# Performance work log

Hardware: AMD Instinct MI355X
Metric: run time of the kernel (lower is better)

The kernel has to match this reference:

```python
import jax, jax.numpy as jnp
import numpy as np

B, H, L, P = 16, 256, 8192, 64  # batch, d_input, seq_len, d_state


def setup_inputs() -> dict:
    key = jax.random.key(0)
    k1, k2, k3, k4, k5, k6 = jax.random.split(key, 6)
    u = jax.random.normal(k1, (B, H, L), dtype=jnp.float32)
    # diagonal SSM poles on an annulus inside the unit disk (stable discrete dynamics)
    radius = jax.random.uniform(k2, (P,), minval=0.5, maxval=0.99)
    theta = jax.random.uniform(k3, (P,), minval=0.0, maxval=2.0 * np.pi)
    A_re = (radius * jnp.cos(theta)).astype(jnp.float32)
    A_im = (radius * jnp.sin(theta)).astype(jnp.float32)
    # combined input/output mixing W = C*B, complex (H, P)
    BC_re = (jax.random.normal(k4, (H, P)) / np.sqrt(P)).astype(jnp.float32)
    BC_im = (jax.random.normal(k5, (H, P)) / np.sqrt(P)).astype(jnp.float32)
    # D skip vector: uniform_ring(min_radius=0.0, max_radius=1.0, field='real')
    D = jax.random.uniform(k6, (H,), minval=0.0, maxval=1.0, dtype=jnp.float32)
    return {"u": u, "A_re": A_re, "A_im": A_im, "BC_re": BC_re, "BC_im": BC_im, "D": D}


def reference(u, A_re, A_im, BC_re, BC_im, D):
    # Vandermonde kernel: k[h, l] = sum_p BC[h, p] * A[p]**l, computed stably via exp(l*log A)
    A = jax.lax.complex(A_re, A_im)                      # (P,)
    logA = jnp.log(A)                                    # (P,) complex
    ell = jnp.arange(L, dtype=jnp.float32)               # (L,)
    V = jnp.exp(logA[:, None] * ell[None, :])            # (P, L) complex Vandermonde
    BC = jax.lax.complex(BC_re, BC_im)                   # (H, P)
    k = jnp.einsum('hp,pl->hl', BC, V)                   # (H, L) complex kernel
    # circular FFT convolution (same-length fft/ifft as the torch code)
    u_s = jnp.fft.fft(u, axis=-1)                        # (B, H, L) complex
    k_s = jnp.fft.fft(k, axis=-1)                        # (H, L) complex
    y = jnp.fft.ifft(u_s * k_s[None, :, :], axis=-1).real
    y = y + D[None, :, None] * u                         # D*u skip
    return jnp.tanh(y)                                   # activation (dropout=0 -> identity)
```

## Files before the change

### kernel.cpp

```cpp
#include <hip/hip_runtime.h>
#include <cmath>


typedef _Float16 half8 __attribute__((ext_vector_type(8)));
typedef _Float16 half4v __attribute__((ext_vector_type(4)));
typedef float floatx16 __attribute__((ext_vector_type(16)));

#define NC 64
#define CM 128
#define A2_BYTES ((size_t)256 * 128 * 256 * 2)
#define W_BYTES  ((size_t)128 * 128 * 2)
#define AM_OFF   (A2_BYTES + W_BYTES)

#define SWH(r, c) ((((r) << 7)) | ((c) ^ (((r) & 15) << 3)))

__device__ __forceinline__ float fast_tanh(float x) {
    float e2 = __expf(2.0f * x);
    return 1.0f - 2.0f / (e2 + 1.0f);
}

__global__ void fftconv_prep(const float* __restrict__ A_re, const float* __restrict__ A_im,
                             const float* __restrict__ BC_re, const float* __restrict__ BC_im,
                             const float* __restrict__ Dv, char* __restrict__ ws) {
    __shared__ float rr[64], th[64], br[64], bi[64];
    __shared__ float kk[CM];
    const int h = blockIdx.x, tid = threadIdx.x;
    if (tid < 64) {
        float x = A_re[tid], y = A_im[tid];
        rr[tid] = log2f(sqrtf(x * x + y * y));
        th[tid] = atan2f(y, x);
        br[tid] = BC_re[h * 64 + tid];
        bi[tid] = BC_im[h * 64 + tid];
    }
    __syncthreads();
    if (tid < CM) {
        float d = (float)tid, s = 0.f;
        for (int p = 0; p < 64; ++p) {
            float mag = exp2f(d * rr[p]);
            float ang = d * th[p];
            s += mag * (br[p] * cosf(ang) - bi[p] * sinf(ang));
        }
        kk[tid] = s;
    }
    __syncthreads();
    _Float16* A2 = (_Float16*)ws + (size_t)h * 128 * 256;
    const float Dh = Dv[h];
    for (int idx = tid; idx < 128 * 128; idx += 256) {
        int r = idx >> 7, pc = idx & 127, p = pc & 63;
        float e = (float)(r + 1);
        float mag = exp2f(e * rr[p]);
        float ang = e * th[p];
        float cr = mag * cosf(ang), ci = mag * sinf(ang);
        float val = (pc < 64) ? (br[p] * cr - bi[p] * ci) : -(br[p] * ci + bi[p] * cr);
        A2[r * 256 + pc] = (_Float16)val;
    }
    for (int idx = tid; idx < 128 * 128; idx += 256) {
        int r = idx >> 7, j = idx & 127;
        float v = (j <= r) ? kk[r - j] : 0.f;
        if (j == r) v += Dh;
        A2[r * 256 + CM + j] = (_Float16)v;
    }
    if (h == 0) {
        _Float16* W = (_Float16*)(ws + A2_BYTES);
        for (int idx = tid; idx < 128 * 128; idx += 256) {
            int pc = idx >> 7, j = idx & 127, p = pc & 63;
            float e = (float)(127 - j);
            float mag = exp2f(e * rr[p]);
            float ang = e * th[p];
            float v = (pc < 64) ? mag * cosf(ang) : mag * sinf(ang);
            W[pc * 128 + j] = (_Float16)v;
        }
        if (tid < 64) {
            float mag = exp2f(128.f * rr[tid]);
            float ang = 128.f * th[tid];
            float* aM = (float*)(ws + AM_OFF);
            aM[tid] = mag * cosf(ang);
            aM[64 + tid] = mag * sinf(ang);
        }
    }
}

__global__ __launch_bounds__(256, 4)
void fftconv_main(const float* __restrict__ u, const char* __restrict__ ws,
                  float* __restrict__ out) {
    __shared__ __align__(16) _Float16 u16[NC * CM];
    __shared__ __align__(16) _Float16 S16[NC * CM];

    const int tid = threadIdx.x;
    const int lane = tid & 63;
    const int wv = tid >> 6;
    const int h = blockIdx.x >> 4;
    const int bb = blockIdx.x & 15;
    const float* ub = u + ((size_t)bb * 256 + h) * 8192;
    float* yb = out + ((size_t)bb * 256 + h) * 8192;

    const int mrow = (wv << 5) + (lane & 31);
    const int kh = (lane >> 5) << 3;
    const int ncol = lane & 31;

    const _Float16* Wg = (const _Float16*)(ws + A2_BYTES) + (size_t)mrow * CM + kh;
    const _Float16* Ag = (const _Float16*)ws + ((size_t)h * CM + mrow) * 256 + kh;

    float4 uv[8];
#pragma unroll
    for (int i = 0; i < 8; ++i) uv[i] = ((const float4*)ub)[i * 256 + tid];
    half8 wf[8];
#pragma unroll
    for (int s = 0; s < 8; ++s) wf[s] = *(const half8*)(Wg + (s << 4));

#pragma unroll
    for (int i = 0; i < 8; ++i) {
        int e4 = i * 256 + tid;
        int c = e4 >> 5, j = (e4 << 2) & 127;
        half4v hv = { (_Float16)uv[i].x, (_Float16)uv[i].y,
                      (_Float16)uv[i].z, (_Float16)uv[i].w };
        *(half4v*)&u16[SWH(c, j)] = hv;
    }
    __syncthreads();

    {
        floatx16 acc0 = {}; floatx16 acc1 = {};
#pragma unroll
        for (int s = 0; s < 8; ++s) {
            int k0 = (s << 4) + kh;
            half8 b0 = *(const half8*)&u16[SWH(ncol, k0)];
            half8 b1 = *(const half8*)&u16[SWH(ncol + 32, k0)];
            acc0 = __builtin_amdgcn_mfma_f32_32x32x16_f16(wf[s], b0, acc0, 0, 0, 0);
            acc1 = __builtin_amdgcn_mfma_f32_32x32x16_f16(wf[s], b1, acc1, 0, 0, 0);
        }
        const int pc0 = (wv << 5) + ((lane >> 5) << 2);
#pragma unroll
        for (int g = 0; g < 4; ++g) {
            half4v h0 = { (_Float16)acc0[4 * g + 0], (_Float16)acc0[4 * g + 1],
                          (_Float16)acc0[4 * g + 2], (_Float16)acc0[4 * g + 3] };
            *(half4v*)&S16[SWH(ncol, pc0 + 8 * g)] = h0;
            half4v h1 = { (_Float16)acc1[4 * g + 0], (_Float16)acc1[4 * g + 1],
                          (_Float16)acc1[4 * g + 2], (_Float16)acc1[4 * g + 3] };
            *(half4v*)&S16[SWH(ncol + 32, pc0 + 8 * g)] = h1;
        }
    }
    half8 gf[8];
#pragma unroll
    for (int s = 0; s < 8; ++s) gf[s] = *(const half8*)(Ag + (s << 4));
    __syncthreads();

    {
        const float* aM = (const float*)(ws + AM_OFF);
        const float amr = aM[lane], ami = aM[64 + lane];
        float prd[8], pid[8];
        prd[0] = 1.f; pid[0] = 0.f;
#pragma unroll
        for (int d = 1; d < 8; ++d) {
            prd[d] = prd[d - 1] * amr - pid[d - 1] * ami;
            pid[d] = prd[d - 1] * ami + pid[d - 1] * amr;
        }
        const int cbase = wv << 4;
        float sr = 0.f, si = 0.f;
#pragma unroll
        for (int d = 0; d < 8; ++d) {
            int cc = (cbase - 1 - d) & 63;
            float xr = (float)S16[SWH(cc, lane)];
            float xi = (float)S16[SWH(cc, 64 + lane)];
            sr = fmaf(prd[d], xr, fmaf(-pid[d], xi, sr));
            si = fmaf(prd[d], xi, fmaf(pid[d], xr, si));
        }
        float er[16], ei[16];
        er[0] = sr; ei[0] = si;
#pragma unroll
        for (int i = 1; i < 16; ++i) {
            int cc = cbase + i - 1;
            float xr = (float)S16[SWH(cc, lane)];
            float xi = (float)S16[SWH(cc, 64 + lane)];
            float nr = fmaf(amr, sr, fmaf(-ami, si, xr));
            float ni = fmaf(amr, si, fmaf(ami, sr, xi));
            sr = nr; si = ni; er[i] = sr; ei[i] = si;
        }
        __syncthreads();
#pragma unroll
        for (int i = 0; i < 16; ++i) {
            int c = cbase + i;
            S16[SWH(c, lane)] = (_Float16)er[i];
            S16[SWH(c, 64 + lane)] = (_Float16)ei[i];
        }
    }
    half8 tf[8];
#pragma unroll
    for (int s = 0; s < 8; ++s) tf[s] = *(const half8*)(Ag + CM + (s << 4));
    __syncthreads();

    {
        floatx16 acc0 = {}; floatx16 acc1 = {};
#pragma unroll
        for (int s = 0; s < 8; ++s) {
            int k0 = (s << 4) + kh;
            half8 b0 = *(const half8*)&S16[SWH(ncol, k0)];
            half8 b1 = *(const half8*)&S16[SWH(ncol + 32, k0)];
            acc0 = __builtin_amdgcn_mfma_f32_32x32x16_f16(gf[s], b0, acc0, 0, 0, 0);
            acc1 = __builtin_amdgcn_mfma_f32_32x32x16_f16(gf[s], b1, acc1, 0, 0, 0);
        }
#pragma unroll
        for (int s = 0; s < 8; ++s) {
            int k0 = (s << 4) + kh;
            half8 b0 = *(const half8*)&u16[SWH(ncol, k0)];
            half8 b1 = *(const half8*)&u16[SWH(ncol + 32, k0)];
            acc0 = __builtin_amdgcn_mfma_f32_32x32x16_f16(tf[s], b0, acc0, 0, 0, 0);
            acc1 = __builtin_amdgcn_mfma_f32_32x32x16_f16(tf[s], b1, acc1, 0, 0, 0);
        }
        const int r0 = (wv << 5) + ((lane >> 5) << 2);
#pragma unroll
        for (int g = 0; g < 4; ++g) {
            float4 o0;
            o0.x = fast_tanh(acc0[4 * g + 0]); o0.y = fast_tanh(acc0[4 * g + 1]);
            o0.z = fast_tanh(acc0[4 * g + 2]); o0.w = fast_tanh(acc0[4 * g + 3]);
            *(float4*)(yb + (size_t)ncol * CM + r0 + 8 * g) = o0;
            float4 o1;
            o1.x = fast_tanh(acc1[4 * g + 0]); o1.y = fast_tanh(acc1[4 * g + 1]);
            o1.z = fast_tanh(acc1[4 * g + 2]); o1.w = fast_tanh(acc1[4 * g + 3]);
            *(float4*)(yb + (size_t)(ncol + 32) * CM + r0 + 8 * g) = o1;
        }
    }
}

extern "C" void kernel_launch(void* const* d_in, const int* in_sizes, int n_in,
                              void* d_out, int out_size, void* d_ws, size_t ws_size,
                              hipStream_t stream) {
    const float* u     = (const float*)d_in[0];
    const float* A_re  = (const float*)d_in[1];
    const float* A_im  = (const float*)d_in[2];
    const float* BC_re = (const float*)d_in[3];
    const float* BC_im = (const float*)d_in[4];
    const float* Dv    = (const float*)d_in[5];
    float* out = (float*)d_out;
    char* ws = (char*)d_ws;

    hipLaunchKernelGGL(fftconv_prep, dim3(256), dim3(256), 0, stream,
                       A_re, A_im, BC_re, BC_im, Dv, ws);
    hipLaunchKernelGGL(fftconv_main, dim3(4096), dim3(256), 0, stream,
                       u, ws, out);
}
```

Baseline: 333.9 us.

## Interleave real/imag state layout and overlap Toeplitz MFMA with chunk scan

Reorders the state columns in the W and A2 precomputed matrices so the real and imaginary parts of each pole sit next to each other. The scan can then read and write them as one half2 LDS access instead of two scalar ones. The direct Toeplitz MFMA (tf times u) now runs before and interleaved with the sequential per-chunk recurrence, so matrix work hides the scan's dependent-FMA latency. The tf prefetch moves earlier and the pole powers are computed on the fly, which raises register pressure from the live accumulators and the er/ei arrays under the 4-waves launch bound.

```diff
diff --git a/kernel.cpp b/kernel.cpp
--- a/kernel.cpp
+++ b/kernel.cpp
@@ -4,6 +4,7 @@
 
 typedef _Float16 half8 __attribute__((ext_vector_type(8)));
 typedef _Float16 half4v __attribute__((ext_vector_type(4)));
+typedef _Float16 half2v __attribute__((ext_vector_type(2)));
 typedef float floatx16 __attribute__((ext_vector_type(16)));
 
 #define NC 64
@@ -52,7 +53,8 @@
         float ang = e * th[p];
         float cr = mag * cosf(ang), ci = mag * sinf(ang);
         float val = (pc < 64) ? (br[p] * cr - bi[p] * ci) : -(br[p] * ci + bi[p] * cr);
-        A2[r * 256 + pc] = (_Float16)val;
+        int cn = ((pc & 63) << 1) | (pc >> 6);
+        A2[r * 256 + cn] = (_Float16)val;
     }
     for (int idx = tid; idx < 128 * 128; idx += 256) {
         int r = idx >> 7, j = idx & 127;
@@ -68,7 +70,8 @@
             float mag = exp2f(e * rr[p]);
             float ang = e * th[p];
             float v = (pc < 64) ? mag * cosf(ang) : mag * sinf(ang);
-            W[pc * 128 + j] = (_Float16)v;
+            int rn = ((pc & 63) << 1) | (pc >> 6);
+            W[rn * 128 + j] = (_Float16)v;
         }
         if (tid < 64) {
             float mag = exp2f(128.f * rr[tid]);
@@ -116,6 +119,9 @@
                       (_Float16)uv[i].z, (_Float16)uv[i].w };
         *(half4v*)&u16[SWH(c, j)] = hv;
     }
+    half8 tf[8];
+#pragma unroll
+    for (int s = 0; s < 8; ++s) tf[s] = *(const half8*)(Ag + CM + (s << 4));
     __syncthreads();
 
     {
@@ -139,83 +145,79 @@
             *(half4v*)&S16[SWH(ncol + 32, pc0 + 8 * g)] = h1;
         }
     }
-    half8 gf[8];
-#pragma unroll
-    for (int s = 0; s < 8; ++s) gf[s] = *(const half8*)(Ag + (s << 4));
-    __syncthreads();
-
+    __syncthreads();
+
+    floatx16 y0 = {}; floatx16 y1 = {};
+    float er[16], ei[16];
     {
         const float* aM = (const float*)(ws + AM_OFF);
         const float amr = aM[lane], ami = aM[64 + lane];
-        float prd[8], pid[8];
-        prd[0] = 1.f; pid[0] = 0.f;
-#pragma unroll
-        for (int d = 1; d < 8; ++d) {
-            prd[d] = prd[d - 1] * amr - pid[d - 1] * ami;
-            pid[d] = prd[d - 1] * ami + pid[d - 1] * amr;
-        }
         const int cbase = wv << 4;
-        float sr = 0.f, si = 0.f;
+        float sr = 0.f, si = 0.f, pr = 1.f, pi = 0.f;
 #pragma unroll
         for (int d = 0; d < 8; ++d) {
             int cc = (cbase - 1 - d) & 63;
-            float xr = (float)S16[SWH(cc, lane)];
-            float xi = (float)S16[SWH(cc, 64 + lane)];
-            sr = fmaf(prd[d], xr, fmaf(-pid[d], xi, sr));
-            si = fmaf(prd[d], xi, fmaf(pid[d], xr, si));
-        }
-        float er[16], ei[16];
+            half2v xv = *(const half2v*)&S16[SWH(cc, lane << 1)];
+            float xr = (float)xv.x, xi = (float)xv.y;
+            sr = fmaf(pr, xr, fmaf(-pi, xi, sr));
+            si = fmaf(pr, xi, fmaf(pi, xr, si));
+            float npr = pr * amr - pi * ami;
+            float npi = pr * ami + pi * amr;
+            pr = npr; pi = npi;
+        }
         er[0] = sr; ei[0] = si;
 #pragma unroll
-        for (int i = 1; i < 16; ++i) {
-            int cc = cbase + i - 1;
-            float xr = (float)S16[SWH(cc, lane)];
-            float xi = (float)S16[SWH(cc, 64 + lane)];
-            float nr = fmaf(amr, sr, fmaf(-ami, si, xr));
-            float ni = fmaf(amr, si, fmaf(ami, sr, xi));
-            sr = nr; si = ni; er[i] = sr; ei[i] = si;
-        }
-        __syncthreads();
-#pragma unroll
-        for (int i = 0; i < 16; ++i) {
-            int c = cbase + i;
-            S16[SWH(c, lane)] = (_Float16)er[i];
-            S16[SWH(c, 64 + lane)] = (_Float16)ei[i];
-        }
-    }
-    half8 tf[8];
-#pragma unroll
-    for (int s = 0; s < 8; ++s) tf[s] = *(const half8*)(Ag + CM + (s << 4));
+        for (int s = 0; s < 8; ++s) {
+            int k0 = (s << 4) + kh;
+            half8 b0 = *(const half8*)&u16[SWH(ncol, k0)];
+            half8 b1 = *(const half8*)&u16[SWH(ncol + 32, k0)];
+            y0 = __builtin_amdgcn_mfma_f32_32x32x16_f16(tf[s], b0, y0, 0, 0, 0);
+            y1 = __builtin_amdgcn_mfma_f32_32x32x16_f16(tf[s], b1, y1, 0, 0, 0);
+#pragma unroll
+            for (int t = 1; t <= 2; ++t) {
+                int i = 2 * s + t;
+                if (i < 16) {
+                    half2v xv = *(const half2v*)&S16[SWH(cbase + i - 1, lane << 1)];
+                    float xr = (float)xv.x, xi = (float)xv.y;
+                    er[i] = fmaf(amr, er[i - 1], fmaf(-ami, ei[i - 1], xr));
+                    ei[i] = fmaf(amr, ei[i - 1], fmaf(ami, er[i - 1], xi));
+                }
+            }
+        }
+    }
+    __syncthreads();
+
+    half8 gf[8];
+#pragma unroll
+    for (int s = 0; s < 8; ++s) gf[s] = *(const half8*)(Ag + (s << 4));
+
+#pragma unroll
+    for (int i = 0; i < 16; ++i) {
+        int c = (wv << 4) + i;
+        half2v ev = { (_Float16)er[i], (_Float16)ei[i] };
+        *(half2v*)&S16[SWH(c, lane << 1)] = ev;
+    }
     __syncthreads();
 
     {
-        floatx16 acc0 = {}; floatx16 acc1 = {};
 #pragma unroll
         for (int s = 0; s < 8; ++s) {
             int k0 = (s << 4) + kh;
             half8 b0 = *(const half8*)&S16[SWH(ncol, k0)];
             half8 b1 = *(const half8*)&S16[SWH(ncol + 32, k0)];
-            acc0 = __builtin_amdgcn_mfma_f32_32x32x16_f16(gf[s], b0, acc0, 0, 0, 0);
-            acc1 = __builtin_amdgcn_mfma_f32_32x32x16_f16(gf[s], b1, acc1, 0, 0, 0);
-        }
-#pragma unroll
-        for (int s = 0; s < 8; ++s) {
-            int k0 = (s << 4) + kh;
-            half8 b0 = *(const half8*)&u16[SWH(ncol, k0)];
-            half8 b1 = *(const half8*)&u16[SWH(ncol + 32, k0)];
-            acc0 = __builtin_amdgcn_mfma_f32_32x32x16_f16(tf[s], b0, acc0, 0, 0, 0);
-            acc1 = __builtin_amdgcn_mfma_f32_32x32x16_f16(tf[s], b1, acc1, 0, 0, 0);
+            y0 = __builtin_amdgcn_mfma_f32_32x32x16_f16(gf[s], b0, y0, 0, 0, 0);
+            y1 = __builtin_amdgcn_mfma_f32_32x32x16_f16(gf[s], b1, y1, 0, 0, 0);
         }
         const int r0 = (wv << 5) + ((lane >> 5) << 2);
 #pragma unroll
         for (int g = 0; g < 4; ++g) {
             float4 o0;
-            o0.x = fast_tanh(acc0[4 * g + 0]); o0.y = fast_tanh(acc0[4 * g + 1]);
-            o0.z = fast_tanh(acc0[4 * g + 2]); o0.w = fast_tanh(acc0[4 * g + 3]);
+            o0.x = fast_tanh(y0[4 * g + 0]); o0.y = fast_tanh(y0[4 * g + 1]);
+            o0.z = fast_tanh(y0[4 * g + 2]); o0.w = fast_tanh(y0[4 * g + 3]);
             *(float4*)(yb + (size_t)ncol * CM + r0 + 8 * g) = o0;
             float4 o1;
-            o1.x = fast_tanh(acc1[4 * g + 0]); o1.y = fast_tanh(acc1[4 * g + 1]);
-            o1.z = fast_tanh(acc1[4 * g + 2]); o1.w = fast_tanh(acc1[4 * g + 3]);
+            o1.x = fast_tanh(y1[4 * g + 0]); o1.y = fast_tanh(y1[4 * g + 1]);
+            o1.z = fast_tanh(y1[4 * g + 2]); o1.w = fast_tanh(y1[4 * g + 3]);
             *(float4*)(yb + (size_t)(ncol + 32) * CM + r0 + 8 * g) = o1;
         }
     }
```

Result: slower. 342.1 us (+2.4%).
